# Kernel optimization log

Hardware: AMD Instinct MI355X
Metric: run time of the kernel (lower is better)

Reference implementation:

```python
import jax, jax.numpy as jnp
import numpy as np

N_NODES = 100000
N_EDGES = 1600000
IN_DIM = 64
OUT_DIM = 64


def setup_inputs() -> dict:
    key = jax.random.key(0)
    k_x, k_e, k_wm, k_bm, k_wu, k_bu = jax.random.split(key, 6)
    x = jax.random.normal(k_x, (N_NODES, IN_DIM), dtype=jnp.float32)
    edge_index = jax.random.randint(k_e, (2, N_EDGES), 0, N_NODES, dtype=jnp.int64)
    # PyTorch Linear default init: U(-1/sqrt(fan_in), 1/sqrt(fan_in))
    lim_m = 1.0 / np.sqrt(2 * IN_DIM)
    lim_u = 1.0 / np.sqrt(IN_DIM + OUT_DIM)
    W_msg = jax.random.uniform(k_wm, (2 * IN_DIM, OUT_DIM), jnp.float32, -lim_m, lim_m)
    b_msg = jax.random.uniform(k_bm, (OUT_DIM,), jnp.float32, -lim_m, lim_m)
    W_upd = jax.random.uniform(k_wu, (IN_DIM + OUT_DIM, OUT_DIM), jnp.float32, -lim_u, lim_u)
    b_upd = jax.random.uniform(k_bu, (OUT_DIM,), jnp.float32, -lim_u, lim_u)
    return {"x": x, "edge_index": edge_index, "W_msg": W_msg, "b_msg": b_msg,
            "W_upd": W_upd, "b_upd": b_upd}


def reference(x, edge_index, W_msg, b_msg, W_upd, b_upd):
    num_nodes = x.shape[0]
    source, target = edge_index[0], edge_index[1]
    # gather endpoint features and compute messages: [E, 2*in] -> [E, out]
    edge_feats = jnp.concatenate([x[source], x[target]], axis=-1)
    messages = jax.nn.relu(edge_feats @ W_msg + b_msg)
    # mean aggregation onto target nodes
    agg_sum = jax.ops.segment_sum(messages, target, num_segments=num_nodes)
    counts = jax.ops.segment_sum(jnp.ones_like(target, dtype=x.dtype), target,
                                 num_segments=num_nodes)
    aggregated = agg_sum / jnp.clip(counts, 1.0, None)[:, None]
    # update MLP: [N, in+out] -> [N, out]
    updated = jax.nn.relu(jnp.concatenate([x, aggregated], axis=-1) @ W_upd + b_upd)
    return updated
```

## Files before the change

kernel.cpp:

```cpp
#include <hip/hip_runtime.h>
#include <hip/hip_bf16.h>

#define N_NODES 100000
#define N_EDGES 1600000
#define DIM 64
#define NB 196
#define CAP 9216
#define SMASK 0x1FFFFu
#define PBLOCKS 391
#define TBLOCKS 1563

typedef __attribute__((ext_vector_type(8))) short bf16x8;
typedef __attribute__((ext_vector_type(4))) float f32x4;
typedef __attribute__((ext_vector_type(2))) float f32x2;

__device__ __forceinline__ unsigned short f2bs(float f) {
    __hip_bfloat16 h = __float2bfloat16(f);
    return *reinterpret_cast<unsigned short*>(&h);
}

__global__ __launch_bounds__(256) void transform_partition(
    const float* __restrict__ x, const float* __restrict__ W_msg,
    const float* __restrict__ b_msg,
    unsigned int* __restrict__ Xs8, unsigned int* __restrict__ Xt8,
    const int* __restrict__ eidx, int* __restrict__ bcursor,
    unsigned int* __restrict__ pairs)
{
    __shared__ __align__(16) char smem[35200];
    const int tid = threadIdx.x, lane = tid & 63, wid = tid >> 6;

    if (blockIdx.x >= PBLOCKS) {
        unsigned short* WB = reinterpret_cast<unsigned short*>(smem);
        const int tb = blockIdx.x - PBLOCKS;

        for (int i = tid; i < 8192; i += 256) {
            const int j = i & 7, l = (i >> 3) & 63, kk = (i >> 9) & 1, ct = i >> 10;
            const int k = kk * 32 + ((l >> 4) << 3) + j;
            const int c = ct * 16 + (l & 15);
            WB[i] = f2bs(W_msg[(((c >> 6) << 6) + k) * 64 + (c & 63)]);
        }
        __syncthreads();

        const int r0 = tb * 64 + wid * 16;
        if (r0 >= N_NODES) return;

        f32x4 acc[8];
        #pragma unroll
        for (int ct = 0; ct < 8; ++ct) acc[ct] = (f32x4){0.f, 0.f, 0.f, 0.f};

        const int r = r0 + (lane & 15);
        #pragma unroll
        for (int kk = 0; kk < 2; ++kk) {
            const int off = kk * 32 + ((lane >> 4) << 3);
            const float4* xp = reinterpret_cast<const float4*>(&x[r * 64 + off]);
            const float4 p0 = xp[0], p1 = xp[1];
            bf16x8 a;
            a[0] = (short)f2bs(p0.x); a[1] = (short)f2bs(p0.y);
            a[2] = (short)f2bs(p0.z); a[3] = (short)f2bs(p0.w);
            a[4] = (short)f2bs(p1.x); a[5] = (short)f2bs(p1.y);
            a[6] = (short)f2bs(p1.z); a[7] = (short)f2bs(p1.w);
            #pragma unroll
            for (int ct = 0; ct < 8; ++ct) {
                const bf16x8 b = *reinterpret_cast<const bf16x8*>(
                    &WB[(((ct << 1) | kk) * 64 + lane) << 3]);
                acc[ct] = __builtin_amdgcn_mfma_f32_16x16x32_bf16(a, b, acc[ct], 0, 0, 0);
            }
        }

        const int fr = lane & 15;
        const int rb = r0 + ((lane >> 4) << 2);
        const float bj0 = b_msg[fr],      bj1 = b_msg[16 + fr];
        const float bj2 = b_msg[32 + fr], bj3 = b_msg[48 + fr];
        #pragma unroll
        for (int q = 0; q < 4; ++q) {
            unsigned int xs = 0;
            xs = (unsigned)__builtin_amdgcn_cvt_pk_fp8_f32(acc[0][q], acc[1][q], (int)xs, false);
            xs = (unsigned)__builtin_amdgcn_cvt_pk_fp8_f32(acc[2][q], acc[3][q], (int)xs, true);
            Xs8[(rb + q) * 16 + fr] = xs;
            unsigned int xt = 0;
            xt = (unsigned)__builtin_amdgcn_cvt_pk_fp8_f32(acc[4][q] + bj0, acc[5][q] + bj1, (int)xt, false);
            xt = (unsigned)__builtin_amdgcn_cvt_pk_fp8_f32(acc[6][q] + bj2, acc[7][q] + bj3, (int)xt, true);
            Xt8[(rb + q) * 16 + fr] = xt;
        }
    } else {
        unsigned int* sbuf = reinterpret_cast<unsigned int*>(smem);
        int* dbase = reinterpret_cast<int*>(smem + 16384);
        int* tcnt  = reinterpret_cast<int*>(smem + 32768);
        int* toff  = tcnt + NB;
        int* gpos  = toff + NB;
        int* wsum  = gpos + NB;

        const int base = blockIdx.x * 4096;
        const int tcount = min(4096, N_EDGES - base);
        if (tid < NB) tcnt[tid] = 0;
        __syncthreads();

        unsigned int pk[16]; int bb[16]; int rk[16];
        #pragma unroll
        for (int j = 0; j < 16; ++j) {
            const int idx = base + j * 256 + tid;
            bb[j] = -1;
            if (idx < N_EDGES) {
                const int sv = eidx[idx];
                const int tv = eidx[N_EDGES + idx];
                bb[j] = tv >> 9;
                pk[j] = (unsigned)sv | ((unsigned)(tv & 511) << 17);
                rk[j] = atomicAdd(&tcnt[bb[j]], 1);
            }
        }
        __syncthreads();

        const int v = (tid < NB) ? tcnt[tid] : 0;
        int s = v;
        #pragma unroll
        for (int d = 1; d < 64; d <<= 1) { int u = __shfl_up(s, d); if (lane >= d) s += u; }
        if (lane == 63) wsum[wid] = s;
        __syncthreads();
        if (wid == 0) {
            int ws = (lane < 4) ? wsum[lane] : 0;
            #pragma unroll
            for (int d = 1; d < 4; d <<= 1) { int u = __shfl_up(ws, d); if (lane >= d) ws += u; }
            if (lane < 4) wsum[lane] = ws;
        }
        __syncthreads();
        const int exc = (wid ? wsum[wid - 1] : 0) + s - v;
        if (tid < NB) {
            toff[tid] = exc;
            gpos[tid] = tid * CAP + (v ? atomicAdd(&bcursor[tid], v) : 0);
        }
        __syncthreads();

        #pragma unroll
        for (int j = 0; j < 16; ++j) {
            if (bb[j] >= 0) {
                const int l = toff[bb[j]] + rk[j];
                sbuf[l]  = pk[j];
                dbase[l] = gpos[bb[j]] + rk[j];
            }
        }
        __syncthreads();
        for (int i = tid; i < tcount; i += 256)
            pairs[dbase[i]] = sbuf[i];
    }
}

__global__ __launch_bounds__(512) void bucket_sort(const int* __restrict__ bcursor,
                                                   const unsigned int* __restrict__ pairs,
                                                   int* __restrict__ csr,
                                                   int* __restrict__ deg,
                                                   int* __restrict__ row)
{
    __shared__ unsigned int ebuf[CAP];
    __shared__ unsigned short rbuf[CAP];
    __shared__ int ncnt[512], noff[512];
    __shared__ int wsum[8];
    const int tid = threadIdx.x, lane = tid & 63, wid = tid >> 6;
    const int b = blockIdx.x;
    const int s0 = b * CAP;
    const int cnt = bcursor[b];
    ncnt[tid] = 0;
    __syncthreads();

    for (int i = tid; i < cnt; i += 512) {
        const unsigned int p = pairs[s0 + i];
        ebuf[i] = p;
        rbuf[i] = (unsigned short)atomicAdd(&ncnt[p >> 17], 1);
    }
    __syncthreads();

    const int v = ncnt[tid];
    int s = v;
    #pragma unroll
    for (int d = 1; d < 64; d <<= 1) { int u = __shfl_up(s, d); if (lane >= d) s += u; }
    if (lane == 63) wsum[wid] = s;
    __syncthreads();
    if (wid == 0) {
        int ws = (lane < 8) ? wsum[lane] : 0;
        #pragma unroll
        for (int d = 1; d < 8; d <<= 1) { int u = __shfl_up(ws, d); if (lane >= d) ws += u; }
        if (lane < 8) wsum[lane] = ws;
    }
    __syncthreads();
    const int exc = (wid ? wsum[wid - 1] : 0) + s - v;
    noff[tid] = exc;
    const int n = b * 512 + tid;
    if (n < N_NODES) { deg[n] = v; row[n] = s0 + exc; }
    __syncthreads();

    for (int i = tid; i < cnt; i += 512) {
        const unsigned int p = ebuf[i];
        csr[s0 + noff[p >> 17] + (int)rbuf[i]] = (int)(p & SMASK);
    }
}

__device__ __forceinline__ void acc_fp8(unsigned int u,
    float t0, float t1, float t2, float t3,
    float& a0, float& a1, float& a2, float& a3)
{
    const f32x2 lo = __builtin_amdgcn_cvt_pk_f32_fp8(u, false);
    const f32x2 hi = __builtin_amdgcn_cvt_pk_f32_fp8(u, true);
    a0 += fmaxf(lo.x + t0, 0.f);
    a1 += fmaxf(lo.y + t1, 0.f);
    a2 += fmaxf(hi.x + t2, 0.f);
    a3 += fmaxf(hi.y + t3, 0.f);
}

__global__ __launch_bounds__(256) void aggregate(
    const int* __restrict__ row, const int* __restrict__ deg,
    const int* __restrict__ csr,
    const unsigned int* __restrict__ Xs8, const unsigned int* __restrict__ Xt8,
    unsigned int* __restrict__ agg8)
{
    const int n = blockIdx.x * 4 + (threadIdx.x >> 6);
    const int lane = threadIdx.x & 63;
    if (n >= N_NODES) return;
    const int c = lane & 15, q = lane >> 4;
    const int start = row[n], d = deg[n];
    const unsigned int tp = Xt8[n * 16 + c];
    const f32x2 tlo = __builtin_amdgcn_cvt_pk_f32_fp8(tp, false);
    const f32x2 thi = __builtin_amdgcn_cvt_pk_f32_fp8(tp, true);
    const float t0 = tlo.x, t1 = tlo.y, t2 = thi.x, t3 = thi.y;
    float a0 = 0.f, a1 = 0.f, a2 = 0.f, a3 = 0.f;

    if (d > 0) {
        int i = 0;
        for (; i + 32 <= d; i += 32) {
            int sv[8];
            #pragma unroll
            for (int k = 0; k < 8; ++k) sv[k] = csr[start + i + 4 * k + q];
            unsigned int u[8];
            #pragma unroll
            for (int k = 0; k < 8; ++k) u[k] = Xs8[sv[k] * 16 + c];
            #pragma unroll
            for (int k = 0; k < 8; ++k) acc_fp8(u[k], t0, t1, t2, t3, a0, a1, a2, a3);
        }
        const int rem = d - i;
        if (rem > 0) {
            const int lastIdx = start + d - 1;
            int sv[8]; bool vm[8];
            #pragma unroll
            for (int k = 0; k < 8; ++k) {
                const int e = i + 4 * k + q;
                vm[k] = (e < d);
                sv[k] = csr[vm[k] ? (start + e) : lastIdx];
            }
            unsigned int u[8];
            #pragma unroll
            for (int k = 0; k < 8; ++k) u[k] = Xs8[sv[k] * 16 + c];
            #pragma unroll
            for (int k = 0; k < 8; ++k) {
                const f32x2 lo = __builtin_amdgcn_cvt_pk_f32_fp8(u[k], false);
                const f32x2 hi = __builtin_amdgcn_cvt_pk_f32_fp8(u[k], true);
                if (vm[k]) {
                    a0 += fmaxf(lo.x + t0, 0.f);
                    a1 += fmaxf(lo.y + t1, 0.f);
                    a2 += fmaxf(hi.x + t2, 0.f);
                    a3 += fmaxf(hi.y + t3, 0.f);
                }
            }
        }
    }

    a0 += __shfl_xor(a0, 16); a0 += __shfl_xor(a0, 32);
    a1 += __shfl_xor(a1, 16); a1 += __shfl_xor(a1, 32);
    a2 += __shfl_xor(a2, 16); a2 += __shfl_xor(a2, 32);
    a3 += __shfl_xor(a3, 16); a3 += __shfl_xor(a3, 32);
    if (q == 0) {
        const float inv = (d > 0) ? 1.0f / (float)d : 0.f;
        unsigned int v = 0;
        v = (unsigned)__builtin_amdgcn_cvt_pk_fp8_f32(a0 * inv, a1 * inv, (int)v, false);
        v = (unsigned)__builtin_amdgcn_cvt_pk_fp8_f32(a2 * inv, a3 * inv, (int)v, true);
        agg8[n * 16 + c] = v;
    }
}

__global__ __launch_bounds__(256) void node_update(
    const float* __restrict__ x, const unsigned int* __restrict__ agg8,
    const float* __restrict__ W_upd, const float* __restrict__ b_upd,
    float* __restrict__ out)
{
    __shared__ unsigned short WB[8192];
    const int tid = threadIdx.x;
    for (int i = tid; i < 8192; i += 256) {
        const int j = i & 7, l = (i >> 3) & 63, kk = (i >> 9) & 3, ct = i >> 11;
        const int hi = l >> 4;
        int k;
        if (kk < 2) k = kk * 32 + (hi << 3) + j;
        else        k = 64 + ((j & 3) << 4) + ((kk - 2) << 3) + (hi << 1) + (j >> 2);
        const int c = ct * 16 + (l & 15);
        WB[i] = f2bs(W_upd[k * 64 + c]);
    }
    __syncthreads();

    const int lane = tid & 63, w = tid >> 6;
    const int r0 = blockIdx.x * 64 + w * 16;
    if (r0 >= N_NODES) return;

    f32x4 acc[4];
    #pragma unroll
    for (int ct = 0; ct < 4; ++ct) acc[ct] = (f32x4){0.f, 0.f, 0.f, 0.f};

    const int fr = lane & 15, hi = lane >> 4;
    const int r = r0 + fr;
    #pragma unroll
    for (int kk = 0; kk < 4; ++kk) {
        bf16x8 a;
        if (kk < 2) {
            const float4* xp = reinterpret_cast<const float4*>(
                &x[r * 64 + kk * 32 + (hi << 3)]);
            const float4 p0 = xp[0], p1 = xp[1];
            a[0] = (short)f2bs(p0.x); a[1] = (short)f2bs(p0.y);
            a[2] = (short)f2bs(p0.z); a[3] = (short)f2bs(p0.w);
            a[4] = (short)f2bs(p1.x); a[5] = (short)f2bs(p1.y);
            a[6] = (short)f2bs(p1.z); a[7] = (short)f2bs(p1.w);
        } else {
            const int off = ((kk - 2) << 3) + (hi << 1);
            const unsigned int u0 = agg8[r * 16 + off];
            const unsigned int u1 = agg8[r * 16 + off + 1];
            const f32x2 l0 = __builtin_amdgcn_cvt_pk_f32_fp8(u0, false);
            const f32x2 h0 = __builtin_amdgcn_cvt_pk_f32_fp8(u0, true);
            const f32x2 l1 = __builtin_amdgcn_cvt_pk_f32_fp8(u1, false);
            const f32x2 h1 = __builtin_amdgcn_cvt_pk_f32_fp8(u1, true);
            a[0] = (short)f2bs(l0.x); a[1] = (short)f2bs(l0.y);
            a[2] = (short)f2bs(h0.x); a[3] = (short)f2bs(h0.y);
            a[4] = (short)f2bs(l1.x); a[5] = (short)f2bs(l1.y);
            a[6] = (short)f2bs(h1.x); a[7] = (short)f2bs(h1.y);
        }
        #pragma unroll
        for (int ct = 0; ct < 4; ++ct) {
            const bf16x8 b = *reinterpret_cast<const bf16x8*>(
                &WB[(((ct << 2) | kk) * 64 + lane) << 3]);
            acc[ct] = __builtin_amdgcn_mfma_f32_16x16x32_bf16(a, b, acc[ct], 0, 0, 0);
        }
    }

    const int rb = r0 + (hi << 2);
    #pragma unroll
    for (int ct = 0; ct < 4; ++ct) {
        const int cc = ct * 16 + fr;
        const float bj = b_upd[cc];
        #pragma unroll
        for (int qq = 0; qq < 4; ++qq)
            out[(rb + qq) * 64 + cc] = fmaxf(acc[ct][qq] + bj, 0.f);
    }
}

extern "C" void kernel_launch(void* const* d_in, const int* in_sizes, int n_in,
                              void* d_out, int out_size, void* d_ws, size_t ws_size,
                              hipStream_t stream) {
    const float* x     = (const float*)d_in[0];
    const int*   eidx  = (const int*)  d_in[1];
    const float* W_msg = (const float*)d_in[2];
    const float* b_msg = (const float*)d_in[3];
    const float* W_upd = (const float*)d_in[4];
    const float* b_upd = (const float*)d_in[5];
    float* out = (float*)d_out;

    int* deg     = (int*)d_ws;
    int* row     = deg + N_NODES;
    int* bcursor = row + N_NODES;
    unsigned int* pairs = (unsigned int*)(bcursor + 256);
    int* csr     = (int*)(pairs + NB * CAP);
    unsigned int* Xs8 = (unsigned int*)(csr + NB * CAP);
    unsigned int* Xt8 = Xs8 + (size_t)N_NODES * 16;
    unsigned int* agg8 = Xt8 + (size_t)N_NODES * 16;

    hipMemsetAsync(bcursor, 0, NB * sizeof(int), stream);
    transform_partition<<<PBLOCKS + TBLOCKS, 256, 0, stream>>>(
        x, W_msg, b_msg, Xs8, Xt8, eidx, bcursor, pairs);
    bucket_sort<<<NB, 512, 0, stream>>>(bcursor, pairs, csr, deg, row);
    aggregate<<<(N_NODES + 3) / 4, 256, 0, stream>>>(row, deg, csr, Xs8, Xt8, agg8);
    node_update<<<(N_NODES + 63) / 64, 256, 0, stream>>>(x, agg8, W_upd, b_upd, out);
}
```

Before: 110.8 us.

## Fuse aggregation with node update MLP and prepack update weights once

Merges the aggregate and node_update kernels so each 1024-thread block averages messages for 16 nodes, keeps the aggregates in shared memory as bf16, and runs the update MFMA directly from there. This removes the agg8 round trip through global memory and one kernel launch. W_upd is converted to bf16 MFMA fragment layout once by an extra block in the transform kernel and copied into LDS per block. bucket_sort also moves to 1024 threads. The cost is that only 4 of 16 waves do the MFMA step, and the large block adds barrier and occupancy limits.

```diff
diff --git a/kernel.cpp b/kernel.cpp
--- a/kernel.cpp
+++ b/kernel.cpp
@@ -24,12 +24,23 @@
     const float* __restrict__ b_msg,
     unsigned int* __restrict__ Xs8, unsigned int* __restrict__ Xt8,
     const int* __restrict__ eidx, int* __restrict__ bcursor,
-    unsigned int* __restrict__ pairs)
+    unsigned int* __restrict__ pairs,
+    const float* __restrict__ W_upd, unsigned short* __restrict__ wfrag)
 {
     __shared__ __align__(16) char smem[35200];
     const int tid = threadIdx.x, lane = tid & 63, wid = tid >> 6;
 
-    if (blockIdx.x >= PBLOCKS) {
+    if (blockIdx.x >= PBLOCKS + TBLOCKS) {
+        for (int i = tid; i < 8192; i += 256) {
+            const int j = i & 7, l = (i >> 3) & 63, kk = (i >> 9) & 3, ct = i >> 11;
+            const int hi = l >> 4;
+            int k;
+            if (kk < 2) k = kk * 32 + (hi << 3) + j;
+            else        k = 64 + ((j & 3) << 4) + ((kk - 2) << 3) + (hi << 1) + (j >> 2);
+            const int c = ct * 16 + (l & 15);
+            wfrag[i] = f2bs(W_upd[k * 64 + c]);
+        }
+    } else if (blockIdx.x >= PBLOCKS) {
         unsigned short* WB = reinterpret_cast<unsigned short*>(smem);
         const int tb = blockIdx.x - PBLOCKS;
 
@@ -144,11 +155,11 @@
     }
 }
 
-__global__ __launch_bounds__(512) void bucket_sort(const int* __restrict__ bcursor,
-                                                   const unsigned int* __restrict__ pairs,
-                                                   int* __restrict__ csr,
-                                                   int* __restrict__ deg,
-                                                   int* __restrict__ row)
+__global__ __launch_bounds__(1024) void bucket_sort(const int* __restrict__ bcursor,
+                                                    const unsigned int* __restrict__ pairs,
+                                                    int* __restrict__ csr,
+                                                    int* __restrict__ deg,
+                                                    int* __restrict__ row)
 {
     __shared__ unsigned int ebuf[CAP];
     __shared__ unsigned short rbuf[CAP];
@@ -158,21 +169,24 @@
     const int b = blockIdx.x;
     const int s0 = b * CAP;
     const int cnt = bcursor[b];
-    ncnt[tid] = 0;
-    __syncthreads();
-
-    for (int i = tid; i < cnt; i += 512) {
+    if (tid < 512) ncnt[tid] = 0;
+    __syncthreads();
+
+    for (int i = tid; i < cnt; i += 1024) {
         const unsigned int p = pairs[s0 + i];
         ebuf[i] = p;
         rbuf[i] = (unsigned short)atomicAdd(&ncnt[p >> 17], 1);
     }
     __syncthreads();
 
-    const int v = ncnt[tid];
-    int s = v;
-    #pragma unroll
-    for (int d = 1; d < 64; d <<= 1) { int u = __shfl_up(s, d); if (lane >= d) s += u; }
-    if (lane == 63) wsum[wid] = s;
+    int v = 0, s = 0;
+    if (tid < 512) {
+        v = ncnt[tid];
+        s = v;
+        #pragma unroll
+        for (int d = 1; d < 64; d <<= 1) { int u = __shfl_up(s, d); if (lane >= d) s += u; }
+        if (lane == 63) wsum[wid] = s;
+    }
     __syncthreads();
     if (wid == 0) {
         int ws = (lane < 8) ? wsum[lane] : 0;
@@ -181,13 +195,15 @@
         if (lane < 8) wsum[lane] = ws;
     }
     __syncthreads();
-    const int exc = (wid ? wsum[wid - 1] : 0) + s - v;
-    noff[tid] = exc;
-    const int n = b * 512 + tid;
-    if (n < N_NODES) { deg[n] = v; row[n] = s0 + exc; }
-    __syncthreads();
-
-    for (int i = tid; i < cnt; i += 512) {
+    if (tid < 512) {
+        const int exc = (wid ? wsum[wid - 1] : 0) + s - v;
+        noff[tid] = exc;
+        const int n = b * 512 + tid;
+        if (n < N_NODES) { deg[n] = v; row[n] = s0 + exc; }
+    }
+    __syncthreads();
+
+    for (int i = tid; i < cnt; i += 1024) {
         const unsigned int p = ebuf[i];
         csr[s0 + noff[p >> 17] + (int)rbuf[i]] = (int)(p & SMASK);
     }
@@ -205,15 +221,22 @@
     a3 += fmaxf(hi.y + t3, 0.f);
 }
 
-__global__ __launch_bounds__(256) void aggregate(
+__global__ __launch_bounds__(1024, 8) void agg_update(
     const int* __restrict__ row, const int* __restrict__ deg,
     const int* __restrict__ csr,
     const unsigned int* __restrict__ Xs8, const unsigned int* __restrict__ Xt8,
-    unsigned int* __restrict__ agg8)
+    const float* __restrict__ x, const unsigned short* __restrict__ wfrag,
+    const float* __restrict__ b_upd, float* __restrict__ out)
 {
-    const int n = blockIdx.x * 4 + (threadIdx.x >> 6);
-    const int lane = threadIdx.x & 63;
-    if (n >= N_NODES) return;
+    __shared__ unsigned short WB[8192];
+    __shared__ uint2 aggT[16][18];
+
+    const int tid = threadIdx.x, lane = tid & 63, w = tid >> 6;
+    const int n0 = blockIdx.x * 16;
+
+    reinterpret_cast<bf16x8*>(WB)[tid] = reinterpret_cast<const bf16x8*>(wfrag)[tid];
+
+    const int n = n0 + w;
     const int c = lane & 15, q = lane >> 4;
     const int start = row[n], d = deg[n];
     const unsigned int tp = Xt8[n * 16 + c];
@@ -267,81 +290,43 @@
     a3 += __shfl_xor(a3, 16); a3 += __shfl_xor(a3, 32);
     if (q == 0) {
         const float inv = (d > 0) ? 1.0f / (float)d : 0.f;
-        unsigned int v = 0;
-        v = (unsigned)__builtin_amdgcn_cvt_pk_fp8_f32(a0 * inv, a1 * inv, (int)v, false);
-        v = (unsigned)__builtin_amdgcn_cvt_pk_fp8_f32(a2 * inv, a3 * inv, (int)v, true);
-        agg8[n * 16 + c] = v;
-    }
-}
-
-__global__ __launch_bounds__(256) void node_update(
-    const float* __restrict__ x, const unsigned int* __restrict__ agg8,
-    const float* __restrict__ W_upd, const float* __restrict__ b_upd,
-    float* __restrict__ out)
-{
-    __shared__ unsigned short WB[8192];
-    const int tid = threadIdx.x;
-    for (int i = tid; i < 8192; i += 256) {
-        const int j = i & 7, l = (i >> 3) & 63, kk = (i >> 9) & 3, ct = i >> 11;
-        const int hi = l >> 4;
-        int k;
-        if (kk < 2) k = kk * 32 + (hi << 3) + j;
-        else        k = 64 + ((j & 3) << 4) + ((kk - 2) << 3) + (hi << 1) + (j >> 2);
-        const int c = ct * 16 + (l & 15);
-        WB[i] = f2bs(W_upd[k * 64 + c]);
-    }
-    __syncthreads();
-
-    const int lane = tid & 63, w = tid >> 6;
-    const int r0 = blockIdx.x * 64 + w * 16;
-    if (r0 >= N_NODES) return;
-
-    f32x4 acc[4];
-    #pragma unroll
-    for (int ct = 0; ct < 4; ++ct) acc[ct] = (f32x4){0.f, 0.f, 0.f, 0.f};
-
-    const int fr = lane & 15, hi = lane >> 4;
-    const int r = r0 + fr;
-    #pragma unroll
-    for (int kk = 0; kk < 4; ++kk) {
-        bf16x8 a;
-        if (kk < 2) {
-            const float4* xp = reinterpret_cast<const float4*>(
-                &x[r * 64 + kk * 32 + (hi << 3)]);
-            const float4 p0 = xp[0], p1 = xp[1];
-            a[0] = (short)f2bs(p0.x); a[1] = (short)f2bs(p0.y);
-            a[2] = (short)f2bs(p0.z); a[3] = (short)f2bs(p0.w);
-            a[4] = (short)f2bs(p1.x); a[5] = (short)f2bs(p1.y);
-            a[6] = (short)f2bs(p1.z); a[7] = (short)f2bs(p1.w);
-        } else {
-            const int off = ((kk - 2) << 3) + (hi << 1);
-            const unsigned int u0 = agg8[r * 16 + off];
-            const unsigned int u1 = agg8[r * 16 + off + 1];
-            const f32x2 l0 = __builtin_amdgcn_cvt_pk_f32_fp8(u0, false);
-            const f32x2 h0 = __builtin_amdgcn_cvt_pk_f32_fp8(u0, true);
-            const f32x2 l1 = __builtin_amdgcn_cvt_pk_f32_fp8(u1, false);
-            const f32x2 h1 = __builtin_amdgcn_cvt_pk_f32_fp8(u1, true);
-            a[0] = (short)f2bs(l0.x); a[1] = (short)f2bs(l0.y);
-            a[2] = (short)f2bs(h0.x); a[3] = (short)f2bs(h0.y);
-            a[4] = (short)f2bs(l1.x); a[5] = (short)f2bs(l1.y);
-            a[6] = (short)f2bs(h1.x); a[7] = (short)f2bs(h1.y);
-        }
-        #pragma unroll
-        for (int ct = 0; ct < 4; ++ct) {
+        uint2 v2;
+        v2.x = (unsigned)f2bs(a0 * inv) | ((unsigned)f2bs(a1 * inv) << 16);
+        v2.y = (unsigned)f2bs(a2 * inv) | ((unsigned)f2bs(a3 * inv) << 16);
+        aggT[w][c] = v2;
+    }
+    __syncthreads();
+
+    if (w < 4) {
+        const int ct = w;
+        f32x4 acc = (f32x4){0.f, 0.f, 0.f, 0.f};
+        const int fr = lane & 15, hi = lane >> 4;
+        const int r = n0 + fr;
+        #pragma unroll
+        for (int kk = 0; kk < 4; ++kk) {
+            bf16x8 a;
+            if (kk < 2) {
+                const float4* xp = reinterpret_cast<const float4*>(
+                    &x[r * 64 + kk * 32 + (hi << 3)]);
+                const float4 p0 = xp[0], p1 = xp[1];
+                a[0] = (short)f2bs(p0.x); a[1] = (short)f2bs(p0.y);
+                a[2] = (short)f2bs(p0.z); a[3] = (short)f2bs(p0.w);
+                a[4] = (short)f2bs(p1.x); a[5] = (short)f2bs(p1.y);
+                a[6] = (short)f2bs(p1.z); a[7] = (short)f2bs(p1.w);
+            } else {
+                a = *reinterpret_cast<const bf16x8*>(
+                    &aggT[fr][((kk - 2) << 3) + (hi << 1)]);
+            }
             const bf16x8 b = *reinterpret_cast<const bf16x8*>(
                 &WB[(((ct << 2) | kk) * 64 + lane) << 3]);
-            acc[ct] = __builtin_amdgcn_mfma_f32_16x16x32_bf16(a, b, acc[ct], 0, 0, 0);
-        }
-    }
-
-    const int rb = r0 + (hi << 2);
-    #pragma unroll
-    for (int ct = 0; ct < 4; ++ct) {
+            acc = __builtin_amdgcn_mfma_f32_16x16x32_bf16(a, b, acc, 0, 0, 0);
+        }
+        const int rb = n0 + (hi << 2);
         const int cc = ct * 16 + fr;
         const float bj = b_upd[cc];
         #pragma unroll
         for (int qq = 0; qq < 4; ++qq)
-            out[(rb + qq) * 64 + cc] = fmaxf(acc[ct][qq] + bj, 0.f);
+            out[(rb + qq) * 64 + cc] = fmaxf(acc[qq] + bj, 0.f);
     }
 }
 
@@ -359,16 +344,16 @@
     int* deg     = (int*)d_ws;
     int* row     = deg + N_NODES;
     int* bcursor = row + N_NODES;
-    unsigned int* pairs = (unsigned int*)(bcursor + 256);
+    unsigned short* wfrag = (unsigned short*)(bcursor + 256);
+    unsigned int* pairs = (unsigned int*)(wfrag + 8192);
     int* csr     = (int*)(pairs + NB * CAP);
     unsigned int* Xs8 = (unsigned int*)(csr + NB * CAP);
     unsigned int* Xt8 = Xs8 + (size_t)N_NODES * 16;
-    unsigned int* agg8 = Xt8 + (size_t)N_NODES * 16;
 
     hipMemsetAsync(bcursor, 0, NB * sizeof(int), stream);
-    transform_partition<<<PBLOCKS + TBLOCKS, 256, 0, stream>>>(
-        x, W_msg, b_msg, Xs8, Xt8, eidx, bcursor, pairs);
-    bucket_sort<<<NB, 512, 0, stream>>>(bcursor, pairs, csr, deg, row);
-    aggregate<<<(N_NODES + 3) / 4, 256, 0, stream>>>(row, deg, csr, Xs8, Xt8, agg8);
-    node_update<<<(N_NODES + 63) / 64, 256, 0, stream>>>(x, agg8, W_upd, b_upd, out);
-}
+    transform_partition<<<PBLOCKS + TBLOCKS + 1, 256, 0, stream>>>(
+        x, W_msg, b_msg, Xs8, Xt8, eidx, bcursor, pairs, W_upd, wfrag);
+    bucket_sort<<<NB, 1024, 0, stream>>>(bcursor, pairs, csr, deg, row);
+    agg_update<<<N_NODES / 16, 1024, 0, stream>>>(row, deg, csr, Xs8, Xt8,
+                                                  x, wfrag, b_upd, out);
+}
```

Result: faster. 105.4 us (-4.9%).
